# Performance work log

Measured on AMD Instinct MI355X. Metric: run time of the kernel, lower is better.

## Reference

```python
import jax, jax.numpy as jnp
import numpy as np
import math

N_OBS, DIM_IN, DIM_HIDDEN = 2048, 64, 1024
LENGTHSCALE = 1.0


def setup_inputs() -> dict:
    key = jax.random.key(0)
    kx, kw, kb = jax.random.split(key, 3)
    x = jax.random.normal(kx, (N_OBS, DIM_IN), dtype=jnp.float32)
    # buffer w ~ Normal(0, 1/lengthscale), b ~ Uniform(0, 2*pi)
    w = jax.random.normal(kw, (DIM_HIDDEN, DIM_IN), dtype=jnp.float32) / LENGTHSCALE
    b = jax.random.uniform(kb, (DIM_HIDDEN,), dtype=jnp.float32, minval=0.0, maxval=2.0 * math.pi)
    return {"x": x, "w": w, "b": b}


def reference(x, w, b):
    """compute_Ax: analytic jacobian of hidden_features + per-dim Gram matrices.

    hidden h = sqrt(2/K) * cos(x @ w.T + b)
    jacobian J[n,k,d] = -sqrt(2/K) * sin(z[n,k]) * w[k,d]
    A_d[k,l] = (1/n) * sum_n J[n,k,d] * J[n,l,d]
             = (1/n) * (S^T S)[k,l] * w[k,d] * w[l,d],  S = -sqrt(2/K) sin(z)
    Returns A stacked: (dim_in, K, K).
    """
    n = x.shape[0]
    K = w.shape[0]
    scale = math.sqrt(2.0 / K)
    z = x @ w.T + b  # (n, K)
    s = (-scale) * jnp.sin(z)  # (n, K)
    M = (s.T @ s) / n  # (K, K) shared Gram of sin-activations
    # A[d,k,l] = M[k,l] * w[k,d] * w[l,d]
    A = jnp.einsum('kl,kd,ld->dkl', M, w, w)
    return A
```

## Files before the change

kernel.cpp:

```cpp
#include <hip/hip_runtime.h>
#include <math.h>

#define N_OBS   2048
#define DIM_IN  64
#define K_HID   1024
#define NCHUNK  (N_OBS / 64)

typedef unsigned short ushort_t;
typedef __attribute__((ext_vector_type(8))) short bf16x8;
typedef __attribute__((ext_vector_type(4))) float f32x4;

__device__ __forceinline__ ushort_t f2bf(float f) {
    unsigned int u = __float_as_uint(f);
    u += 0x7FFF + ((u >> 16) & 1);
    return (ushort_t)(u >> 16);
}

#define GLD_LDS16(g, l)                                                   \
    __builtin_amdgcn_global_load_lds(                                     \
        (const __attribute__((address_space(1))) void*)(g),               \
        (__attribute__((address_space(3))) void*)(l), 16, 0, 0)

__global__ __launch_bounds__(256) void rff_compute_s(
    const float* __restrict__ x, const float* __restrict__ w,
    const float* __restrict__ b, ushort_t* __restrict__ sT) {
    __shared__ float xs[16][64];
    __shared__ float wT[64][65];

    const int t  = threadIdx.x;
    const int k0 = blockIdx.x * 64;
    const int n0 = blockIdx.y * 16;

    {
        int r = t >> 4, c = (t & 15) * 4;
        *(float4*)&xs[r][c] = *(const float4*)(x + (n0 + r) * DIM_IN + c);
    }
#pragma unroll
    for (int i = 0; i < 4; ++i) {
        int r = (t >> 4) + 16 * i, c = (t & 15) * 4;
        float4 v = *(const float4*)(w + (k0 + r) * DIM_IN + c);
        wT[c + 0][r] = v.x; wT[c + 1][r] = v.y;
        wT[c + 2][r] = v.z; wT[c + 3][r] = v.w;
    }
    __syncthreads();

    const int k  = t & 63;
    const int nb = t >> 6;
    const float bk = b[k0 + k];
    float z[4];
#pragma unroll
    for (int i = 0; i < 4; ++i) z[i] = bk;

    for (int d4 = 0; d4 < 64; d4 += 4) {
        float xv[4][4];
#pragma unroll
        for (int i = 0; i < 4; ++i)
            *(float4*)xv[i] = *(const float4*)&xs[nb * 4 + i][d4];
#pragma unroll
        for (int j = 0; j < 4; ++j) {
            const float wv = wT[d4 + j][k];
#pragma unroll
            for (int i = 0; i < 4; ++i) z[i] += xv[i][j] * wv;
        }
    }

    const float scale = 0.04419417382415922f;
    ushort4 ov;
    ov.x = f2bf(-scale * __sinf(z[0]));
    ov.y = f2bf(-scale * __sinf(z[1]));
    ov.z = f2bf(-scale * __sinf(z[2]));
    ov.w = f2bf(-scale * __sinf(z[3]));
    *(ushort4*)(sT + (size_t)(k0 + k) * N_OBS + n0 + nb * 4) = ov;
}

__device__ __forceinline__ void stage_tiles(
    const ushort_t* __restrict__ sT, ushort_t* buf,
    int k0, int l0, int ncol0, int wv, int srow, int sslot) {
#pragma unroll
    for (int j = 0; j < 2; ++j) {
        const int c = wv * 2 + j;
        const ushort_t* gA = sT + (size_t)(k0 + c * 8 + srow) * N_OBS + ncol0 + sslot * 8;
        const ushort_t* gB = sT + (size_t)(l0 + c * 8 + srow) * N_OBS + ncol0 + sslot * 8;
        GLD_LDS16(gA, buf + c * 512);
        GLD_LDS16(gB, buf + 4096 + c * 512);
    }
}

__global__ __launch_bounds__(256) void rff_gram_expand(
    const ushort_t* __restrict__ sT, const float* __restrict__ w,
    float* __restrict__ out) {
    __shared__ __align__(16) char smem[52224];
    ushort_t* stg   = (ushort_t*)smem;
    float*    M_lds = (float*)smem;
    float*    wkT   = (float*)(smem + 17408);
    float*    wlT   = (float*)(smem + 34816);

    const int t    = threadIdx.x;
    const int lane = t & 63;
    const int wv   = t >> 6;
    const int wr   = wv >> 1, wc = wv & 1;
    const int k0   = blockIdx.y * 64, l0 = blockIdx.x * 64;

    const int srow  = lane >> 3;
    const int sslot = (lane & 7) ^ srow;

    f32x4 acc[2][2];
#pragma unroll
    for (int a = 0; a < 2; ++a)
#pragma unroll
        for (int bb = 0; bb < 2; ++bb)
            acc[a][bb] = (f32x4){0.f, 0.f, 0.f, 0.f};

    const int rlo = lane & 15;
    const int hi  = lane >> 4;
    const int rx  = rlo & 7;

    stage_tiles(sT, stg,        k0, l0,  0, wv, srow, sslot);
    stage_tiles(sT, stg + 8192, k0, l0, 64, wv, srow, sslot);

    for (int it = 0; it < NCHUNK; ++it) {
        if (it == NCHUNK - 1) {
            asm volatile("s_waitcnt vmcnt(0)" ::: "memory");
        } else {
            asm volatile("s_waitcnt vmcnt(4)" ::: "memory");
        }
        __builtin_amdgcn_s_barrier();
        if (it + 2 < NCHUNK)
            stage_tiles(sT, stg + ((it + 2) % 3) * 8192,
                        k0, l0, (it + 2) * 64, wv, srow, sslot);
        const ushort_t* bufA = stg + (it % 3) * 8192;
        const ushort_t* bufB = bufA + 4096;
#pragma unroll
        for (int ks = 0; ks < 2; ++ks) {
            const int slot = (ks * 4 + hi) ^ rx;
            bf16x8 af[2], bfr[2];
#pragma unroll
            for (int a = 0; a < 2; ++a) {
                af[a]  = *(const bf16x8*)(bufA + (wr * 32 + a * 16 + rlo) * 64 + slot * 8);
                bfr[a] = *(const bf16x8*)(bufB + (wc * 32 + a * 16 + rlo) * 64 + slot * 8);
            }
#pragma unroll
            for (int a = 0; a < 2; ++a)
#pragma unroll
                for (int bb = 0; bb < 2; ++bb)
                    acc[a][bb] = __builtin_amdgcn_mfma_f32_16x16x32_bf16(
                        af[a], bfr[bb], acc[a][bb], 0, 0, 0);
        }
    }
    __syncthreads();

    const float inv_n = 1.0f / (float)N_OBS;
    const int col = lane & 15;
    const int rq  = (lane >> 4) * 4;
#pragma unroll
    for (int a = 0; a < 2; ++a)
#pragma unroll
        for (int bb = 0; bb < 2; ++bb)
#pragma unroll
            for (int r = 0; r < 4; ++r) {
                const int row = wr * 32 + a * 16 + rq + r;
                const int cl  = wc * 32 + bb * 16 + col;
                M_lds[row * 68 + cl] = acc[a][bb][r] * inv_n;
            }
#pragma unroll
    for (int i = 0; i < 4; ++i) {
        const int r = (t >> 4) + 16 * i, c = (t & 15) * 4;
        float4 vk = *(const float4*)(w + (k0 + r) * DIM_IN + c);
        float4 vl = *(const float4*)(w + (l0 + r) * DIM_IN + c);
        wkT[(c + 0) * 68 + r] = vk.x; wkT[(c + 1) * 68 + r] = vk.y;
        wkT[(c + 2) * 68 + r] = vk.z; wkT[(c + 3) * 68 + r] = vk.w;
        wlT[(c + 0) * 68 + r] = vl.x; wlT[(c + 1) * 68 + r] = vl.y;
        wlT[(c + 2) * 68 + r] = vl.z; wlT[(c + 3) * 68 + r] = vl.w;
    }
    __syncthreads();

    const int prow = t >> 4;
    const int pcol = (t & 15) * 4;
    f32x4 mv[4];
#pragma unroll
    for (int rr = 0; rr < 4; ++rr)
        mv[rr] = *(const f32x4*)&M_lds[(rr * 16 + prow) * 68 + pcol];

    float* outb = out + (size_t)k0 * K_HID + l0;
#pragma unroll 2
    for (int d = 0; d < DIM_IN; ++d) {
        const f32x4 wlv = *(const f32x4*)&wlT[d * 68 + pcol];
        float* outd = outb + (size_t)d * K_HID * K_HID;
#pragma unroll
        for (int rr = 0; rr < 4; ++rr) {
            const int row = rr * 16 + prow;
            const float wk = wkT[d * 68 + row];
            f32x4 o;
#pragma unroll
            for (int j = 0; j < 4; ++j) o[j] = mv[rr][j] * wk * wlv[j];
            __builtin_nontemporal_store(
                o, (f32x4*)(outd + (size_t)row * K_HID + pcol));
        }
    }
}

extern "C" void kernel_launch(void* const* d_in, const int* in_sizes, int n_in,
                              void* d_out, int out_size, void* d_ws, size_t ws_size,
                              hipStream_t stream) {
    const float* x = (const float*)d_in[0];
    const float* w = (const float*)d_in[1];
    const float* b = (const float*)d_in[2];
    float* out = (float*)d_out;

    ushort_t* sT_buf = (ushort_t*)d_ws;

    rff_compute_s<<<dim3(K_HID / 64, N_OBS / 16), 256, 0, stream>>>(x, w, b, sT_buf);
    rff_gram_expand<<<dim3(K_HID / 64, K_HID / 64), 256, 0, stream>>>(sT_buf, w, out);
}
```

Before: 291.1 us.

## Double gram_expand block to 512 threads, splitting MFMA and store work across eight waves

The Gram/expand kernel now runs 512 threads (8 waves) per 64x64 output tile instead of 256. Each wave computes a 32x16 sub-tile with two MFMAs per k-step, staging uses one load pair per wave, and the expand phase has each thread write two rows instead of four. The goal is more waves in flight to hide latency in the store-bound 268 MB output write and the MFMA loop. The trade-off is more barrier participants and possibly lower per-wave MFMA operand reuse.

```diff
diff --git a/kernel.cpp b/kernel.cpp
--- a/kernel.cpp
+++ b/kernel.cpp
@@ -76,17 +76,13 @@
 __device__ __forceinline__ void stage_tiles(
     const ushort_t* __restrict__ sT, ushort_t* buf,
     int k0, int l0, int ncol0, int wv, int srow, int sslot) {
-#pragma unroll
-    for (int j = 0; j < 2; ++j) {
-        const int c = wv * 2 + j;
-        const ushort_t* gA = sT + (size_t)(k0 + c * 8 + srow) * N_OBS + ncol0 + sslot * 8;
-        const ushort_t* gB = sT + (size_t)(l0 + c * 8 + srow) * N_OBS + ncol0 + sslot * 8;
-        GLD_LDS16(gA, buf + c * 512);
-        GLD_LDS16(gB, buf + 4096 + c * 512);
-    }
-}
-
-__global__ __launch_bounds__(256) void rff_gram_expand(
+    const ushort_t* gA = sT + (size_t)(k0 + wv * 8 + srow) * N_OBS + ncol0 + sslot * 8;
+    const ushort_t* gB = sT + (size_t)(l0 + wv * 8 + srow) * N_OBS + ncol0 + sslot * 8;
+    GLD_LDS16(gA, buf + wv * 512);
+    GLD_LDS16(gB, buf + 4096 + wv * 512);
+}
+
+__global__ __launch_bounds__(512, 2) void rff_gram_expand(
     const ushort_t* __restrict__ sT, const float* __restrict__ w,
     float* __restrict__ out) {
     __shared__ __align__(16) char smem[52224];
@@ -98,18 +94,16 @@
     const int t    = threadIdx.x;
     const int lane = t & 63;
     const int wv   = t >> 6;
-    const int wr   = wv >> 1, wc = wv & 1;
+    const int wr   = wv >> 2, wc = wv & 3;
     const int k0   = blockIdx.y * 64, l0 = blockIdx.x * 64;
 
     const int srow  = lane >> 3;
     const int sslot = (lane & 7) ^ srow;
 
-    f32x4 acc[2][2];
+    f32x4 acc[2];
 #pragma unroll
     for (int a = 0; a < 2; ++a)
-#pragma unroll
-        for (int bb = 0; bb < 2; ++bb)
-            acc[a][bb] = (f32x4){0.f, 0.f, 0.f, 0.f};
+        acc[a] = (f32x4){0.f, 0.f, 0.f, 0.f};
 
     const int rlo = lane & 15;
     const int hi  = lane >> 4;
@@ -122,7 +116,7 @@
         if (it == NCHUNK - 1) {
             asm volatile("s_waitcnt vmcnt(0)" ::: "memory");
         } else {
-            asm volatile("s_waitcnt vmcnt(4)" ::: "memory");
+            asm volatile("s_waitcnt vmcnt(2)" ::: "memory");
         }
         __builtin_amdgcn_s_barrier();
         if (it + 2 < NCHUNK)
@@ -133,18 +127,15 @@
 #pragma unroll
         for (int ks = 0; ks < 2; ++ks) {
             const int slot = (ks * 4 + hi) ^ rx;
-            bf16x8 af[2], bfr[2];
-#pragma unroll
-            for (int a = 0; a < 2; ++a) {
-                af[a]  = *(const bf16x8*)(bufA + (wr * 32 + a * 16 + rlo) * 64 + slot * 8);
-                bfr[a] = *(const bf16x8*)(bufB + (wc * 32 + a * 16 + rlo) * 64 + slot * 8);
-            }
+            bf16x8 af[2], bfr;
 #pragma unroll
             for (int a = 0; a < 2; ++a)
-#pragma unroll
-                for (int bb = 0; bb < 2; ++bb)
-                    acc[a][bb] = __builtin_amdgcn_mfma_f32_16x16x32_bf16(
-                        af[a], bfr[bb], acc[a][bb], 0, 0, 0);
+                af[a] = *(const bf16x8*)(bufA + (wr * 32 + a * 16 + rlo) * 64 + slot * 8);
+            bfr = *(const bf16x8*)(bufB + (wc * 16 + rlo) * 64 + slot * 8);
+#pragma unroll
+            for (int a = 0; a < 2; ++a)
+                acc[a] = __builtin_amdgcn_mfma_f32_16x16x32_bf16(
+                    af[a], bfr, acc[a], 0, 0, 0);
         }
     }
     __syncthreads();
@@ -155,16 +146,14 @@
 #pragma unroll
     for (int a = 0; a < 2; ++a)
 #pragma unroll
-        for (int bb = 0; bb < 2; ++bb)
-#pragma unroll
-            for (int r = 0; r < 4; ++r) {
-                const int row = wr * 32 + a * 16 + rq + r;
-                const int cl  = wc * 32 + bb * 16 + col;
-                M_lds[row * 68 + cl] = acc[a][bb][r] * inv_n;
-            }
-#pragma unroll
-    for (int i = 0; i < 4; ++i) {
-        const int r = (t >> 4) + 16 * i, c = (t & 15) * 4;
+        for (int r = 0; r < 4; ++r) {
+            const int row = wr * 32 + a * 16 + rq + r;
+            const int cl  = wc * 16 + col;
+            M_lds[row * 68 + cl] = acc[a][r] * inv_n;
+        }
+#pragma unroll
+    for (int i = 0; i < 2; ++i) {
+        const int r = (t >> 4) + 32 * i, c = (t & 15) * 4;
         float4 vk = *(const float4*)(w + (k0 + r) * DIM_IN + c);
         float4 vl = *(const float4*)(w + (l0 + r) * DIM_IN + c);
         wkT[(c + 0) * 68 + r] = vk.x; wkT[(c + 1) * 68 + r] = vk.y;
@@ -174,28 +163,29 @@
     }
     __syncthreads();
 
-    const int prow = t >> 4;
-    const int pcol = (t & 15) * 4;
-    f32x4 mv[4];
-#pragma unroll
-    for (int rr = 0; rr < 4; ++rr)
-        mv[rr] = *(const f32x4*)&M_lds[(rr * 16 + prow) * 68 + pcol];
+    const int trow = t >> 4;
+    const int tcol = (t & 15) * 4;
+    f32x4 mv[2];
+    mv[0] = *(const f32x4*)&M_lds[trow * 68 + tcol];
+    mv[1] = *(const f32x4*)&M_lds[(trow + 32) * 68 + tcol];
 
     float* outb = out + (size_t)k0 * K_HID + l0;
 #pragma unroll 2
     for (int d = 0; d < DIM_IN; ++d) {
-        const f32x4 wlv = *(const f32x4*)&wlT[d * 68 + pcol];
+        const f32x4 wlv = *(const f32x4*)&wlT[d * 68 + tcol];
         float* outd = outb + (size_t)d * K_HID * K_HID;
-#pragma unroll
-        for (int rr = 0; rr < 4; ++rr) {
-            const int row = rr * 16 + prow;
-            const float wk = wkT[d * 68 + row];
-            f32x4 o;
-#pragma unroll
-            for (int j = 0; j < 4; ++j) o[j] = mv[rr][j] * wk * wlv[j];
-            __builtin_nontemporal_store(
-                o, (f32x4*)(outd + (size_t)row * K_HID + pcol));
-        }
+        const float wk0 = wkT[d * 68 + trow];
+        const float wk1 = wkT[d * 68 + trow + 32];
+        f32x4 o0, o1;
+#pragma unroll
+        for (int j = 0; j < 4; ++j) {
+            o0[j] = mv[0][j] * wk0 * wlv[j];
+            o1[j] = mv[1][j] * wk1 * wlv[j];
+        }
+        __builtin_nontemporal_store(
+            o0, (f32x4*)(outd + (size_t)trow * K_HID + tcol));
+        __builtin_nontemporal_store(
+            o1, (f32x4*)(outd + (size_t)(trow + 32) * K_HID + tcol));
     }
 }
 
@@ -210,5 +200,5 @@
     ushort_t* sT_buf = (ushort_t*)d_ws;
 
     rff_compute_s<<<dim3(K_HID / 64, N_OBS / 16), 256, 0, stream>>>(x, w, b, sT_buf);
-    rff_gram_expand<<<dim3(K_HID / 64, K_HID / 64), 256, 0, stream>>>(sT_buf, w, out);
-}
+    rff_gram_expand<<<dim3(K_HID / 64, K_HID / 64), 512, 0, stream>>>(sT_buf, w, out);
+}
```

Result: no change. 292.8 us (+0.6%).
